# Optimization experiments

Hardware: AMD Instinct MI355X
Metric: run time of the kernel (lower is better)

Reference implementation:

```python
import jax, jax.numpy as jnp
import numpy as np

N_NODES = 1048576   # 32768 molecules * 32 atoms
N_EDGES = 4194304   # avg degree 4
D = 32              # feature dim (num_atom_typ == layer1 out dim)
R = 4               # num bond types


def setup_inputs() -> dict:
    key = jax.random.key(0)
    ks = jax.random.split(key, 7)
    x = jax.random.normal(ks[0], (N_NODES, D), dtype=jnp.float32)
    W = jax.random.normal(ks[1], (R, D, D), dtype=jnp.float32) * (1.0 / np.sqrt(D))
    W_loop = jax.random.normal(ks[2], (D, D), dtype=jnp.float32) * (1.0 / np.sqrt(D))
    bias = jax.random.normal(ks[3], (D,), dtype=jnp.float32) * 0.02
    src = jax.random.randint(ks[4], (N_EDGES,), 0, N_NODES, dtype=jnp.int32)
    dst = jax.random.randint(ks[5], (N_EDGES,), 0, N_NODES, dtype=jnp.int32)
    etype = jax.random.randint(ks[6], (N_EDGES,), 0, R, dtype=jnp.int32)
    return {"x": x, "W": W, "W_loop": W_loop, "bias": bias,
            "src": src, "dst": dst, "etype": etype, "bs": 32}


def _rel_graph_conv(h, W, W_loop, bias, src, dst, etype):
    # Per-relation projection for all nodes: [N, R, D] (R is tiny, D=32)
    hw = jnp.einsum('ni,rio->nro', h, W)
    # Irregular gather: message for edge e is W[etype[e]] @ h[src[e]]
    msgs = hw[src, etype]  # [E, D]
    # Sum-scatter to destination nodes
    agg = jax.ops.segment_sum(msgs, dst, num_segments=h.shape[0])
    # Self-loop + bias (DGL RelGraphConv defaults)
    return agg + h @ W_loop + bias


def reference(x, W, W_loop, bias, src, dst, etype, bs):
    # Faithful to original: layer1 is applied TWICE (layer2 unused in source)
    h = jax.nn.relu(_rel_graph_conv(x, W, W_loop, bias, src, dst, etype))
    h = jax.nn.relu(_rel_graph_conv(h, W, W_loop, bias, src, dst, etype))
    # x.split(bs, dim=0) + per-chunk mean == reshape to [n_mols, bs, D] + mean
    vs = h.reshape(-1, bs, h.shape[-1]).mean(axis=1)
    return vs
```

## Files before the change

kernel.cpp:

```cpp
#include <hip/hip_runtime.h>
#include <hip/hip_bf16.h>
#include <stdint.h>


__global__ void init_kernel(int* cnt) {
    if (threadIdx.x < 4) cnt[threadIdx.x] = 0;
}

__global__ __launch_bounds__(1024) void hist_kernel(const int* __restrict__ etype, int E,
                                                    int* __restrict__ cnt) {
    __shared__ int h[4];
    if (threadIdx.x < 4) h[threadIdx.x] = 0;
    __syncthreads();
    int e = blockIdx.x * 1024 + threadIdx.x;
    if (e < E) atomicAdd(&h[etype[e] & 3], 1);
    __syncthreads();
    if (threadIdx.x < 4) atomicAdd(&cnt[threadIdx.x], h[threadIdx.x]);
}

__global__ void scan_kernel(const int* __restrict__ cnt, int* __restrict__ off,
                            int* __restrict__ alloc) {
    if (threadIdx.x == 0) {
        int s = 0;
        for (int r = 0; r < 4; ++r) { off[r] = s; alloc[r] = s; s += cnt[r]; }
    }
}

__global__ __launch_bounds__(1024) void scatter_kernel(const int* __restrict__ src,
                                                       const int* __restrict__ dst,
                                                       const int* __restrict__ etype, int E,
                                                       int* __restrict__ alloc,
                                                       int2* __restrict__ bsd) {
    __shared__ int h[4], base[4], pos[4];
    if (threadIdx.x < 4) { h[threadIdx.x] = 0; pos[threadIdx.x] = 0; }
    __syncthreads();
    int e = blockIdx.x * 1024 + threadIdx.x;
    int et = 0;
    bool valid = (e < E);
    if (valid) { et = etype[e] & 3; atomicAdd(&h[et], 1); }
    __syncthreads();
    if (threadIdx.x < 4) base[threadIdx.x] = atomicAdd(&alloc[threadIdx.x], h[threadIdx.x]);
    __syncthreads();
    if (valid) {
        int p = atomicAdd(&pos[et], 1);
        bsd[base[et] + p] = make_int2(src[e], dst[e]);
    }
}

template<bool RELU>
__global__ __launch_bounds__(256) void selfloop_kernel(const float* __restrict__ h,
                                                       const float* __restrict__ Wl,
                                                       const float* __restrict__ bias,
                                                       float* __restrict__ outb, int N) {
    const int co = (threadIdx.x & 15) * 2;
    float2 w[32];
#pragma unroll
    for (int i = 0; i < 32; ++i) w[i] = *(const float2*)(Wl + i * 32 + co);
    const float2 b = *(const float2*)(bias + co);
    int node = (blockIdx.x * 256 + threadIdx.x) >> 4;
    const int stride = (gridDim.x * 256) >> 4;
    for (; node < N; node += stride) {
        const float4* hp = (const float4*)(h + (size_t)node * 32);
        float4 hv[8];
#pragma unroll
        for (int j = 0; j < 8; ++j) {
            float4 v = hp[j];
            if (RELU) {
                v.x = fmaxf(v.x, 0.f); v.y = fmaxf(v.y, 0.f);
                v.z = fmaxf(v.z, 0.f); v.w = fmaxf(v.w, 0.f);
            }
            hv[j] = v;
        }
        float a0 = b.x, a1 = b.y;
#pragma unroll
        for (int j = 0; j < 8; ++j) {
            a0 = fmaf(hv[j].x, w[4*j+0].x, a0); a1 = fmaf(hv[j].x, w[4*j+0].y, a1);
            a0 = fmaf(hv[j].y, w[4*j+1].x, a0); a1 = fmaf(hv[j].y, w[4*j+1].y, a1);
            a0 = fmaf(hv[j].z, w[4*j+2].x, a0); a1 = fmaf(hv[j].z, w[4*j+2].y, a1);
            a0 = fmaf(hv[j].w, w[4*j+3].x, a0); a1 = fmaf(hv[j].w, w[4*j+3].y, a1);
        }
        *(float2*)(outb + (size_t)node * 32 + co) = make_float2(a0, a1);
    }
}

template<bool RELU>
__global__ __launch_bounds__(256) void edge_kernel(const float* __restrict__ h,
                                                   const float* __restrict__ W,
                                                   const int2* __restrict__ bsd,
                                                   const int* __restrict__ off,
                                                   const int* __restrict__ cnt,
                                                   float* __restrict__ agg) {
    const int r   = blockIdx.x & 3;
    const int sub = blockIdx.x >> 2;
    const int co  = (threadIdx.x & 15) * 2;
    const float* Wr = W + r * 1024;
    float2 w[32];
#pragma unroll
    for (int i = 0; i < 32; ++i) w[i] = *(const float2*)(Wr + i * 32 + co);
    const int n    = cnt[r];
    const int base = off[r];
    const int stride = (gridDim.x >> 2) * (256 / 16);
    int i = sub * (256 / 16) + (threadIdx.x >> 4);
    for (; i < n; i += stride) {
        const int2 sd = bsd[base + i];
        const float4* hp = (const float4*)(h + (size_t)sd.x * 32);
        float4 hv[8];
#pragma unroll
        for (int j = 0; j < 8; ++j) {
            float4 v = hp[j];
            if (RELU) {
                v.x = fmaxf(v.x, 0.f); v.y = fmaxf(v.y, 0.f);
                v.z = fmaxf(v.z, 0.f); v.w = fmaxf(v.w, 0.f);
            }
            hv[j] = v;
        }
        float a0 = 0.f, a1 = 0.f;
#pragma unroll
        for (int j = 0; j < 8; ++j) {
            a0 = fmaf(hv[j].x, w[4*j+0].x, a0); a1 = fmaf(hv[j].x, w[4*j+0].y, a1);
            a0 = fmaf(hv[j].y, w[4*j+1].x, a0); a1 = fmaf(hv[j].y, w[4*j+1].y, a1);
            a0 = fmaf(hv[j].z, w[4*j+2].x, a0); a1 = fmaf(hv[j].z, w[4*j+2].y, a1);
            a0 = fmaf(hv[j].w, w[4*j+3].x, a0); a1 = fmaf(hv[j].w, w[4*j+3].y, a1);
        }
        float* outp = agg + (size_t)sd.y * 32 + co;
        atomicAdd(outp,     a0);
        atomicAdd(outp + 1, a1);
    }
}

__global__ __launch_bounds__(256) void pool_kernel(const float* __restrict__ pre2,
                                                   float* __restrict__ out, int total) {
    int t = blockIdx.x * 256 + threadIdx.x;
    if (t >= total) return;
    const int m = t >> 5, o = t & 31;
    const float* p = pre2 + (size_t)m * 1024 + o;
    float s = 0.f;
#pragma unroll
    for (int a = 0; a < 32; ++a) s += fmaxf(p[a * 32], 0.f);
    out[t] = s * (1.0f / 32.0f);
}

extern "C" void kernel_launch(void* const* d_in, const int* in_sizes, int n_in,
                              void* d_out, int out_size, void* d_ws, size_t ws_size,
                              hipStream_t stream) {
    const float* x     = (const float*)d_in[0];
    const float* W     = (const float*)d_in[1];
    const float* Wl    = (const float*)d_in[2];
    const float* bias  = (const float*)d_in[3];
    const int*   src   = (const int*)d_in[4];
    const int*   dst   = (const int*)d_in[5];
    const int*   etype = (const int*)d_in[6];

    const int N = in_sizes[0] / 32;
    const int E = in_sizes[4];
    const int M = N / 32;

    char* ws = (char*)d_ws;
    float* agg1  = (float*)ws;
    float* agg2  = (float*)(ws + (size_t)N * 32 * 4);
    int2*  bsd   = (int2*)(ws + (size_t)N * 32 * 4 * 2);
    int*   cnt   = (int*)(ws + (size_t)N * 32 * 4 * 2 + (size_t)E * 8);
    int*   off   = cnt + 4;
    int*   alloc = cnt + 8;

    const int hb = (E + 1023) / 1024;

    init_kernel<<<1, 64, 0, stream>>>(cnt);
    hist_kernel<<<hb, 1024, 0, stream>>>(etype, E, cnt);
    scan_kernel<<<1, 64, 0, stream>>>(cnt, off, alloc);
    scatter_kernel<<<hb, 1024, 0, stream>>>(src, dst, etype, E, alloc, bsd);

    selfloop_kernel<false><<<8192, 256, 0, stream>>>(x, Wl, bias, agg1, N);
    edge_kernel<false><<<8192, 256, 0, stream>>>(x, W, bsd, off, cnt, agg1);

    selfloop_kernel<true><<<8192, 256, 0, stream>>>(agg1, Wl, bias, agg2, N);
    edge_kernel<true><<<8192, 256, 0, stream>>>(agg1, W, bsd, off, cnt, agg2);

    pool_kernel<<<(M * 32 + 255) / 256, 256, 0, stream>>>(agg2, (float*)d_out, M * 32);
}
```

Baseline: 2.308 ms.

## Build dst-sorted CSR and fuse edge aggregation with self-loop per node

Replaces the relation-bucketed edge list and atomic scatter with a CSR grouped by destination node, built from a histogram, a three-pass scan and an atomic fill. Each conv layer becomes a single pull-style kernel where a wavefront owns a contiguous range of destination nodes, keeps all four relation weights and the self-loop weight in registers, and accumulates messages without float atomics. This removes the separate self-loop pass and the global atomic adds, at the cost of extra CSR build passes, a per-edge branch on relation type, and load imbalance from varying node degrees. The packed column index assumes source ids fit in 28 bits and the scan hardcodes sizes that need N to be a multiple of 1024 with N/1024 at most 1024.

```diff
diff --git a/kernel.cpp b/kernel.cpp
--- a/kernel.cpp
+++ b/kernel.cpp
@@ -3,128 +3,155 @@
 #include <stdint.h>
 
 
-__global__ void init_kernel(int* cnt) {
-    if (threadIdx.x < 4) cnt[threadIdx.x] = 0;
-}
-
-__global__ __launch_bounds__(1024) void hist_kernel(const int* __restrict__ etype, int E,
-                                                    int* __restrict__ cnt) {
-    __shared__ int h[4];
-    if (threadIdx.x < 4) h[threadIdx.x] = 0;
+__global__ __launch_bounds__(256) void zero_kernel(int4* p, int n4) {
+    int i = blockIdx.x * 256 + threadIdx.x;
+    const int st = gridDim.x * 256;
+    for (; i < n4; i += st) p[i] = make_int4(0, 0, 0, 0);
+}
+
+__global__ __launch_bounds__(256) void hist_kernel(const int* __restrict__ dst, int E,
+                                                   int* __restrict__ cnt) {
+    int i = blockIdx.x * 256 + threadIdx.x;
+    const int st = gridDim.x * 256;
+    for (; i < E; i += st) atomicAdd(&cnt[dst[i]], 1);
+}
+
+__global__ __launch_bounds__(256) void scan_a(const int4* __restrict__ cnt4,
+                                              int* __restrict__ partial) {
+    __shared__ int lds[256];
+    const int b = blockIdx.x, t = threadIdx.x;
+    int4 c = cnt4[b * 256 + t];
+    lds[t] = c.x + c.y + c.z + c.w;
     __syncthreads();
-    int e = blockIdx.x * 1024 + threadIdx.x;
-    if (e < E) atomicAdd(&h[etype[e] & 3], 1);
+    for (int off = 128; off > 0; off >>= 1) {
+        if (t < off) lds[t] += lds[t + off];
+        __syncthreads();
+    }
+    if (t == 0) partial[b] = lds[0];
+}
+
+__global__ __launch_bounds__(1024) void scan_b(int* __restrict__ partial) {
+    __shared__ int lds[1024];
+    const int t = threadIdx.x;
+    const int v = partial[t];
+    lds[t] = v;
     __syncthreads();
-    if (threadIdx.x < 4) atomicAdd(&cnt[threadIdx.x], h[threadIdx.x]);
-}
-
-__global__ void scan_kernel(const int* __restrict__ cnt, int* __restrict__ off,
-                            int* __restrict__ alloc) {
-    if (threadIdx.x == 0) {
-        int s = 0;
-        for (int r = 0; r < 4; ++r) { off[r] = s; alloc[r] = s; s += cnt[r]; }
-    }
-}
-
-__global__ __launch_bounds__(1024) void scatter_kernel(const int* __restrict__ src,
-                                                       const int* __restrict__ dst,
-                                                       const int* __restrict__ etype, int E,
-                                                       int* __restrict__ alloc,
-                                                       int2* __restrict__ bsd) {
-    __shared__ int h[4], base[4], pos[4];
-    if (threadIdx.x < 4) { h[threadIdx.x] = 0; pos[threadIdx.x] = 0; }
+    for (int off = 1; off < 1024; off <<= 1) {
+        int add = (t >= off) ? lds[t - off] : 0;
+        __syncthreads();
+        lds[t] += add;
+        __syncthreads();
+    }
+    partial[t] = lds[t] - v;
+}
+
+__global__ __launch_bounds__(256) void scan_c(const int4* __restrict__ cnt4,
+                                              const int* __restrict__ partial,
+                                              int* __restrict__ row_ptr,
+                                              int* __restrict__ fill, int N, int E) {
+    __shared__ int lds[256];
+    const int b = blockIdx.x, t = threadIdx.x;
+    int4 c = cnt4[b * 256 + t];
+    const int s = c.x + c.y + c.z + c.w;
+    lds[t] = s;
     __syncthreads();
-    int e = blockIdx.x * 1024 + threadIdx.x;
-    int et = 0;
-    bool valid = (e < E);
-    if (valid) { et = etype[e] & 3; atomicAdd(&h[et], 1); }
-    __syncthreads();
-    if (threadIdx.x < 4) base[threadIdx.x] = atomicAdd(&alloc[threadIdx.x], h[threadIdx.x]);
-    __syncthreads();
-    if (valid) {
-        int p = atomicAdd(&pos[et], 1);
-        bsd[base[et] + p] = make_int2(src[e], dst[e]);
-    }
-}
+    for (int off = 1; off < 256; off <<= 1) {
+        int add = (t >= off) ? lds[t - off] : 0;
+        __syncthreads();
+        lds[t] += add;
+        __syncthreads();
+    }
+    const int base = partial[b] + lds[t] - s;
+    const int idx = b * 1024 + t * 4;
+    int r0 = base, r1 = r0 + c.x, r2 = r1 + c.y, r3 = r2 + c.z;
+    row_ptr[idx] = r0; row_ptr[idx + 1] = r1;
+    row_ptr[idx + 2] = r2; row_ptr[idx + 3] = r3;
+    fill[idx] = r0; fill[idx + 1] = r1; fill[idx + 2] = r2; fill[idx + 3] = r3;
+    if (b == 0 && t == 0) row_ptr[N] = E;
+}
+
+__global__ __launch_bounds__(256) void fill_kernel(const int* __restrict__ src,
+                                                   const int* __restrict__ dst,
+                                                   const int* __restrict__ etype, int E,
+                                                   int* __restrict__ fill,
+                                                   int* __restrict__ col) {
+    int i = blockIdx.x * 256 + threadIdx.x;
+    const int st = gridDim.x * 256;
+    for (; i < E; i += st) {
+        int d = dst[i];
+        int slot = atomicAdd(&fill[d], 1);
+        col[slot] = ((etype[i] & 3) << 28) | src[i];
+    }
+}
+
+#define RELU4(v) { v.x = fmaxf(v.x, 0.f); v.y = fmaxf(v.y, 0.f); \
+                   v.z = fmaxf(v.z, 0.f); v.w = fmaxf(v.w, 0.f); }
+
+#define MAC16(WA) { \
+    acc = fmaf(v0.x, WA[0],  acc); acc = fmaf(v0.y, WA[1],  acc); \
+    acc = fmaf(v0.z, WA[2],  acc); acc = fmaf(v0.w, WA[3],  acc); \
+    acc = fmaf(v1.x, WA[4],  acc); acc = fmaf(v1.y, WA[5],  acc); \
+    acc = fmaf(v1.z, WA[6],  acc); acc = fmaf(v1.w, WA[7],  acc); \
+    acc = fmaf(v2.x, WA[8],  acc); acc = fmaf(v2.y, WA[9],  acc); \
+    acc = fmaf(v2.z, WA[10], acc); acc = fmaf(v2.w, WA[11], acc); \
+    acc = fmaf(v3.x, WA[12], acc); acc = fmaf(v3.y, WA[13], acc); \
+    acc = fmaf(v3.z, WA[14], acc); acc = fmaf(v3.w, WA[15], acc); }
 
 template<bool RELU>
-__global__ __launch_bounds__(256) void selfloop_kernel(const float* __restrict__ h,
-                                                       const float* __restrict__ Wl,
-                                                       const float* __restrict__ bias,
-                                                       float* __restrict__ outb, int N) {
-    const int co = (threadIdx.x & 15) * 2;
-    float2 w[32];
+__global__ __launch_bounds__(256) void conv_kernel(const float* __restrict__ h,
+                                                   const float* __restrict__ W,
+                                                   const float* __restrict__ Wl,
+                                                   const float* __restrict__ bias,
+                                                   const int* __restrict__ row_ptr,
+                                                   const int* __restrict__ col,
+                                                   float* __restrict__ out, int N) {
+    const int lane = threadIdx.x & 63;
+    const int o = lane & 31;
+    const int ihalf = lane >> 5;
+    const int i0 = ihalf * 16;
+
+    float wr0[16], wr1[16], wr2[16], wr3[16], wl[16];
 #pragma unroll
-    for (int i = 0; i < 32; ++i) w[i] = *(const float2*)(Wl + i * 32 + co);
-    const float2 b = *(const float2*)(bias + co);
-    int node = (blockIdx.x * 256 + threadIdx.x) >> 4;
-    const int stride = (gridDim.x * 256) >> 4;
-    for (; node < N; node += stride) {
-        const float4* hp = (const float4*)(h + (size_t)node * 32);
-        float4 hv[8];
-#pragma unroll
-        for (int j = 0; j < 8; ++j) {
-            float4 v = hp[j];
-            if (RELU) {
-                v.x = fmaxf(v.x, 0.f); v.y = fmaxf(v.y, 0.f);
-                v.z = fmaxf(v.z, 0.f); v.w = fmaxf(v.w, 0.f);
+    for (int ii = 0; ii < 16; ++ii) {
+        wr0[ii] = W[0 * 1024 + (i0 + ii) * 32 + o];
+        wr1[ii] = W[1 * 1024 + (i0 + ii) * 32 + o];
+        wr2[ii] = W[2 * 1024 + (i0 + ii) * 32 + o];
+        wr3[ii] = W[3 * 1024 + (i0 + ii) * 32 + o];
+        wl[ii]  = Wl[(i0 + ii) * 32 + o];
+    }
+    const float bo = bias[o];
+
+    const int wid = (blockIdx.x * 256 + threadIdx.x) >> 6;
+    const int nw = (gridDim.x * 256) >> 6;
+    const int chunk = (N + nw - 1) / nw;
+    const int dbeg = wid * chunk;
+    const int dend = min(N, dbeg + chunk);
+
+    for (int d = dbeg; d < dend; ++d) {
+        const int e0 = row_ptr[d], e1 = row_ptr[d + 1];
+        const float4* hp = (const float4*)(h + (size_t)d * 32 + i0);
+        float4 v0 = hp[0], v1 = hp[1], v2 = hp[2], v3 = hp[3];
+        if (RELU) { RELU4(v0); RELU4(v1); RELU4(v2); RELU4(v3); }
+        float acc = bo;
+        MAC16(wl);
+        int c = (e0 < e1) ? col[e0] : 0;
+        for (int e = e0; e < e1; ++e) {
+            int cn = (e + 1 < e1) ? col[e + 1] : 0;
+            const int r = c >> 28;
+            const int s = c & 0x0FFFFFFF;
+            const float4* sp = (const float4*)(h + (size_t)s * 32 + i0);
+            v0 = sp[0]; v1 = sp[1]; v2 = sp[2]; v3 = sp[3];
+            if (RELU) { RELU4(v0); RELU4(v1); RELU4(v2); RELU4(v3); }
+            switch (r) {
+                case 0:  MAC16(wr0); break;
+                case 1:  MAC16(wr1); break;
+                case 2:  MAC16(wr2); break;
+                default: MAC16(wr3); break;
             }
-            hv[j] = v;
+            c = cn;
         }
-        float a0 = b.x, a1 = b.y;
-#pragma unroll
-        for (int j = 0; j < 8; ++j) {
-            a0 = fmaf(hv[j].x, w[4*j+0].x, a0); a1 = fmaf(hv[j].x, w[4*j+0].y, a1);
-            a0 = fmaf(hv[j].y, w[4*j+1].x, a0); a1 = fmaf(hv[j].y, w[4*j+1].y, a1);
-            a0 = fmaf(hv[j].z, w[4*j+2].x, a0); a1 = fmaf(hv[j].z, w[4*j+2].y, a1);
-            a0 = fmaf(hv[j].w, w[4*j+3].x, a0); a1 = fmaf(hv[j].w, w[4*j+3].y, a1);
-        }
-        *(float2*)(outb + (size_t)node * 32 + co) = make_float2(a0, a1);
-    }
-}
-
-template<bool RELU>
-__global__ __launch_bounds__(256) void edge_kernel(const float* __restrict__ h,
-                                                   const float* __restrict__ W,
-                                                   const int2* __restrict__ bsd,
-                                                   const int* __restrict__ off,
-                                                   const int* __restrict__ cnt,
-                                                   float* __restrict__ agg) {
-    const int r   = blockIdx.x & 3;
-    const int sub = blockIdx.x >> 2;
-    const int co  = (threadIdx.x & 15) * 2;
-    const float* Wr = W + r * 1024;
-    float2 w[32];
-#pragma unroll
-    for (int i = 0; i < 32; ++i) w[i] = *(const float2*)(Wr + i * 32 + co);
-    const int n    = cnt[r];
-    const int base = off[r];
-    const int stride = (gridDim.x >> 2) * (256 / 16);
-    int i = sub * (256 / 16) + (threadIdx.x >> 4);
-    for (; i < n; i += stride) {
-        const int2 sd = bsd[base + i];
-        const float4* hp = (const float4*)(h + (size_t)sd.x * 32);
-        float4 hv[8];
-#pragma unroll
-        for (int j = 0; j < 8; ++j) {
-            float4 v = hp[j];
-            if (RELU) {
-                v.x = fmaxf(v.x, 0.f); v.y = fmaxf(v.y, 0.f);
-                v.z = fmaxf(v.z, 0.f); v.w = fmaxf(v.w, 0.f);
-            }
-            hv[j] = v;
-        }
-        float a0 = 0.f, a1 = 0.f;
-#pragma unroll
-        for (int j = 0; j < 8; ++j) {
-            a0 = fmaf(hv[j].x, w[4*j+0].x, a0); a1 = fmaf(hv[j].x, w[4*j+0].y, a1);
-            a0 = fmaf(hv[j].y, w[4*j+1].x, a0); a1 = fmaf(hv[j].y, w[4*j+1].y, a1);
-            a0 = fmaf(hv[j].z, w[4*j+2].x, a0); a1 = fmaf(hv[j].z, w[4*j+2].y, a1);
-            a0 = fmaf(hv[j].w, w[4*j+3].x, a0); a1 = fmaf(hv[j].w, w[4*j+3].y, a1);
-        }
-        float* outp = agg + (size_t)sd.y * 32 + co;
-        atomicAdd(outp,     a0);
-        atomicAdd(outp + 1, a1);
+        acc += __shfl_xor(acc, 32);
+        if (ihalf == 0) out[(size_t)d * 32 + o] = acc;
     }
 }
 
@@ -156,25 +183,23 @@
     const int M = N / 32;
 
     char* ws = (char*)d_ws;
-    float* agg1  = (float*)ws;
-    float* agg2  = (float*)(ws + (size_t)N * 32 * 4);
-    int2*  bsd   = (int2*)(ws + (size_t)N * 32 * 4 * 2);
-    int*   cnt   = (int*)(ws + (size_t)N * 32 * 4 * 2 + (size_t)E * 8);
-    int*   off   = cnt + 4;
-    int*   alloc = cnt + 8;
-
-    const int hb = (E + 1023) / 1024;
-
-    init_kernel<<<1, 64, 0, stream>>>(cnt);
-    hist_kernel<<<hb, 1024, 0, stream>>>(etype, E, cnt);
-    scan_kernel<<<1, 64, 0, stream>>>(cnt, off, alloc);
-    scatter_kernel<<<hb, 1024, 0, stream>>>(src, dst, etype, E, alloc, bsd);
-
-    selfloop_kernel<false><<<8192, 256, 0, stream>>>(x, Wl, bias, agg1, N);
-    edge_kernel<false><<<8192, 256, 0, stream>>>(x, W, bsd, off, cnt, agg1);
-
-    selfloop_kernel<true><<<8192, 256, 0, stream>>>(agg1, Wl, bias, agg2, N);
-    edge_kernel<true><<<8192, 256, 0, stream>>>(agg1, W, bsd, off, cnt, agg2);
-
-    pool_kernel<<<(M * 32 + 255) / 256, 256, 0, stream>>>(agg2, (float*)d_out, M * 32);
-}
+    float* pre1    = (float*)ws;
+    float* pre2    = (float*)(ws + (size_t)134217728);
+    int*   col     = (int*)(ws + (size_t)268435456);
+    int*   row_ptr = (int*)(ws + (size_t)285212672);
+    int*   fill    = (int*)(ws + (size_t)289407040);
+    int*   cnt     = (int*)(ws + (size_t)293601344);
+    int*   partial = (int*)(ws + (size_t)297795648);
+
+    zero_kernel<<<1024, 256, 0, stream>>>((int4*)cnt, N / 4);
+    hist_kernel<<<4096, 256, 0, stream>>>(dst, E, cnt);
+    scan_a<<<N / 1024, 256, 0, stream>>>((const int4*)cnt, partial);
+    scan_b<<<1, 1024, 0, stream>>>(partial);
+    scan_c<<<N / 1024, 256, 0, stream>>>((const int4*)cnt, partial, row_ptr, fill, N, E);
+    fill_kernel<<<4096, 256, 0, stream>>>(src, dst, etype, E, fill, col);
+
+    conv_kernel<false><<<4096, 256, 0, stream>>>(x,    W, Wl, bias, row_ptr, col, pre1, N);
+    conv_kernel<true ><<<4096, 256, 0, stream>>>(pre1, W, Wl, bias, row_ptr, col, pre2, N);
+
+    pool_kernel<<<(M * 32 + 255) / 256, 256, 0, stream>>>(pre2, (float*)d_out, M * 32);
+}
```

Measured after the change: 3.227 ms. +39.8%, slower.
